# Kernel optimization log

Hardware: AMD Instinct MI355X
Metric: run time of the kernel (lower is better)

Reference implementation:

```python
import jax, jax.numpy as jnp
import numpy as np
from jax import lax

H = 128  # hidden_size


def lstm_last_h(x, w_ih, w_hh, b_ih, b_hh):
    """PyTorch-style single-layer LSTM; returns final hidden state.
    x: (B, T, D). Gate order i, f, g, o. w_ih: (4H, D), w_hh: (4H, H)."""
    B = x.shape[0]
    Hh = w_hh.shape[1]
    x_proj = jnp.einsum('btd,gd->btg', x, w_ih) + b_ih + b_hh  # (B, T, 4H)

    def step(carry, xt):
        h, c = carry
        gates = xt + h @ w_hh.T
        i, f, g, o = jnp.split(gates, 4, axis=-1)
        i = jax.nn.sigmoid(i)
        f = jax.nn.sigmoid(f)
        g = jnp.tanh(g)
        o = jax.nn.sigmoid(o)
        c = f * c + i * g
        h = o * jnp.tanh(c)
        return (h, c), None

    init = (jnp.zeros((B, Hh), x.dtype), jnp.zeros((B, Hh), x.dtype))
    (h, _), _ = lax.scan(step, init, jnp.swapaxes(x_proj, 0, 1))
    return h  # (B, H)


def setup_inputs() -> dict:
    key = jax.random.key(0)
    ks = jax.random.split(key, 12)
    s = 0.05
    return {
        'x_players': jax.random.normal(ks[0], (64, 22, 128, 2), jnp.float32),
        'x_ball': jax.random.normal(ks[1], (64, 128, 2), jnp.float32),
        'p_w_ih': jax.random.normal(ks[2], (4 * H, 2), jnp.float32) * s,
        'p_w_hh': jax.random.normal(ks[3], (4 * H, H), jnp.float32) * s,
        'p_b_ih': jax.random.normal(ks[4], (4 * H,), jnp.float32) * s,
        'p_b_hh': jax.random.normal(ks[5], (4 * H,), jnp.float32) * s,
        'b_w_ih': jax.random.normal(ks[6], (4 * H, 2), jnp.float32) * s,
        'b_w_hh': jax.random.normal(ks[7], (4 * H, H), jnp.float32) * s,
        'b_b_ih': jax.random.normal(ks[8], (4 * H,), jnp.float32) * s,
        'b_b_hh': jax.random.normal(ks[9], (4 * H,), jnp.float32) * s,
        'fc_w': jax.random.normal(ks[10], (40, 2 * H), jnp.float32) * s,
        'fc_b': jax.random.normal(ks[11], (40,), jnp.float32) * s,
    }


def reference(x_players, x_ball, p_w_ih, p_w_hh, p_b_ih, p_b_hh,
              b_w_ih, b_w_hh, b_b_ih, b_b_hh, fc_w, fc_b):
    B, P, T, D = x_players.shape
    ball_h = lstm_last_h(x_ball, b_w_ih, b_w_hh, b_b_ih, b_b_hh)  # (B, H)
    # Shared player LSTM: fold players into batch (replaces per-player loop).
    ph = lstm_last_h(x_players.reshape(B * P, T, D),
                     p_w_ih, p_w_hh, p_b_ih, p_b_hh).reshape(B, P, H)
    ball_rep = jnp.broadcast_to(ball_h[:, None, :], (B, P, H))
    combined = jnp.concatenate([ph, ball_rep], axis=-1)  # (B, P, 2H)
    out = combined @ fc_w.T + fc_b  # (B, P, 40)
    return out.reshape(B, P, 20, 2)
```

## Files before the change

### kernel.cpp

```cpp
#include <hip/hip_runtime.h>


#define HDIM 128
#define TSTEPS 128
#define NPLAYER 1408
#define NSEQ 1472
#define NB 8
#define NBLK (NSEQ / NB)
#define NPBLK (NPLAYER / NB)
#define KT 5
#define BSTR 168
#define XSTR 258
#define HSTR 132

typedef _Float16 f16x8 __attribute__((ext_vector_type(8)));
typedef _Float16 f16x2 __attribute__((ext_vector_type(2)));
typedef float    f32x4 __attribute__((ext_vector_type(4)));

#define LOG2E 1.44269504f

__device__ __forceinline__ float rcp_fast(float x) { return __builtin_amdgcn_rcpf(x); }
__device__ __forceinline__ float sigmoid_f(float x) {
    return rcp_fast(1.0f + __builtin_amdgcn_exp2f(-LOG2E * x));
}
__device__ __forceinline__ float tanh_f(float x) {
    return 1.0f - 2.0f * rcp_fast(__builtin_amdgcn_exp2f(2.0f * LOG2E * x) + 1.0f);
}
__device__ __forceinline__ float dpp_xor8(float x) {
    return __int_as_float(__builtin_amdgcn_update_dpp(
        __float_as_int(x), __float_as_int(x), 0x128, 0xF, 0xF, false));
}

__global__ void __launch_bounds__(512)
__attribute__((amdgpu_waves_per_eu(2, 2)))
lstm_fc_kernel(const float* __restrict__ x_players, const float* __restrict__ x_ball,
               const float* __restrict__ p_w_ih, const float* __restrict__ p_w_hh,
               const float* __restrict__ p_b_ih, const float* __restrict__ p_b_hh,
               const float* __restrict__ b_w_ih, const float* __restrict__ b_w_hh,
               const float* __restrict__ b_b_ih, const float* __restrict__ b_b_hh,
               const float* __restrict__ fc_w, const float* __restrict__ fc_b,
               float* __restrict__ out)
{
    const int tid  = threadIdx.x;
    const int blk  = blockIdx.x;
    const int w    = tid >> 6;
    const int lane = tid & 63;
    const int nn   = lane & 15;
    const int q    = lane >> 4;

    const bool ball = (blk >= NPBLK);
    const float* w_ih = ball ? b_w_ih : p_w_ih;
    const float* w_hh = ball ? b_w_hh : p_w_hh;
    const float* bih  = ball ? b_b_ih : p_b_ih;
    const float* bhh  = ball ? b_b_hh : p_b_hh;
    const float* xg   = ball ? (x_ball    + (size_t)(blk - NPBLK) * NB * TSTEPS * 2)
                             : (x_players + (size_t)blk * NB * TSTEPS * 2);

    __shared__ __align__(16) _Float16 b_sh[2][NB * BSTR];
    __shared__ __align__(16) float x_sh[NB * XSTR];
    __shared__ __align__(16) float hbuf[NB * HSTR];
    __shared__ float vout[NB * 40];

    for (int i = tid; i < NB * 256; i += 512)
        x_sh[(i >> 8) * XSTR + (i & 255)] = xg[i];
    for (int i = tid; i < 2 * NB * BSTR / 2; i += 512)
        ((int*)b_sh)[i] = 0;

    f16x8 afr[4][KT];
    #pragma unroll
    for (int mi = 0; mi < 4; ++mi) {
        const int r = mi * HDIM + w * 16 + nn;
        const float* wr = w_hh + (size_t)r * HDIM;
        #pragma unroll
        for (int kt = 0; kt < 4; ++kt) {
            const float* p = wr + kt * 32 + q * 8;
            f16x8 a8;
            #pragma unroll
            for (int j = 0; j < 8; ++j) a8[j] = (_Float16)p[j];
            afr[mi][kt] = a8;
        }
        f16x8 a8 = {};
        if (q == 0) {
            a8[0] = (_Float16)w_ih[2 * r];
            a8[1] = (_Float16)w_ih[2 * r + 1];
            a8[2] = (_Float16)(bih[r] + bhh[r]);
        }
        afr[mi][4] = a8;
    }

    const int colh   = nn & 7;
    const int rowoff = (nn < 8) ? 0 : 2;
    const int hrow   = w * 16 + 4 * q + rowoff;
    float c0 = 0.f, c1 = 0.f;
    float h0 = 0.f, h1 = 0.f;

    __syncthreads();
    if (tid < NB) {
        _Float16* br0 = &b_sh[0][tid * BSTR];
        br0[128] = (_Float16)x_sh[tid * XSTR];
        br0[129] = (_Float16)x_sh[tid * XSTR + 1];
        br0[130] = (_Float16)1.0f;
        b_sh[1][tid * BSTR + 130] = (_Float16)1.0f;
    }
    __syncthreads();

    f16x8 bfr[KT] = {};

    auto substep = [&](int s, const _Float16* bc, _Float16* bn, bool last) {
        if (nn < 8) {
            #pragma unroll
            for (int kt = 0; kt < KT; ++kt)
                bfr[kt] = *(const f16x8*)(bc + nn * BSTR + kt * 32 + q * 8);
        }

        f32x4 acc[4];
        #pragma unroll
        for (int mi = 0; mi < 4; ++mi) acc[mi] = (f32x4){0.f, 0.f, 0.f, 0.f};
        #pragma unroll
        for (int kt = 0; kt < KT; ++kt)
            #pragma unroll
            for (int mi = 0; mi < 4; ++mi)
                acc[mi] = __builtin_amdgcn_mfma_f32_16x16x32_f16(afr[mi][kt], bfr[kt], acc[mi], 0, 0, 0);

        if (!last && tid < NB) {
            const float x0 = x_sh[tid * XSTR + 2 * (s + 1)];
            const float x1 = x_sh[tid * XSTR + 2 * (s + 1) + 1];
            *(f16x2*)&bn[tid * BSTR + 128] = (f16x2){(_Float16)x0, (_Float16)x1};
        }

        float u0[4], u1[4];
        #pragma unroll
        for (int mi = 0; mi < 4; ++mi) {
            const float r2 = dpp_xor8(acc[mi][2]);
            const float r3 = dpp_xor8(acc[mi][3]);
            u0[mi] = (nn < 8) ? acc[mi][0] : r2;
            u1[mi] = (nn < 8) ? acc[mi][1] : r3;
        }
        const float i0 = sigmoid_f(u0[0]), i1 = sigmoid_f(u1[0]);
        const float f0 = sigmoid_f(u0[1]), f1 = sigmoid_f(u1[1]);
        const float g0 = tanh_f(u0[2]),    g1 = tanh_f(u1[2]);
        const float o0 = sigmoid_f(u0[3]), o1 = sigmoid_f(u1[3]);
        c0 = __builtin_fmaf(f0, c0, i0 * g0);
        c1 = __builtin_fmaf(f1, c1, i1 * g1);
        h0 = o0 * tanh_f(c0);
        h1 = o1 * tanh_f(c1);

        if (!last) {
            *(f16x2*)&bn[colh * BSTR + hrow] = (f16x2){(_Float16)h0, (_Float16)h1};
            __syncthreads();
        }
    };

    _Float16* b0 = &b_sh[0][0];
    _Float16* b1 = &b_sh[1][0];
    #pragma unroll 1
    for (int it = 0; it < TSTEPS / 2 - 1; ++it) {
        substep(2 * it,     b0, b1, false);
        substep(2 * it + 1, b1, b0, false);
        asm volatile("" : "+a"(afr[0][0]), "+a"(afr[0][1]), "+a"(afr[0][2]), "+a"(afr[0][3]), "+a"(afr[0][4]));
        asm volatile("" : "+a"(afr[1][0]), "+a"(afr[1][1]), "+a"(afr[1][2]), "+a"(afr[1][3]), "+a"(afr[1][4]));
        asm volatile("" : "+a"(afr[2][0]), "+a"(afr[2][1]), "+a"(afr[2][2]), "+a"(afr[2][3]), "+a"(afr[2][4]));
        asm volatile("" : "+a"(afr[3][0]), "+a"(afr[3][1]), "+a"(afr[3][2]), "+a"(afr[3][3]), "+a"(afr[3][4]));
    }
    substep(126, b0, b1, false);
    substep(127, b1, b0, true);

    hbuf[colh * HSTR + hrow]     = h0;
    hbuf[colh * HSTR + hrow + 1] = h1;
    __syncthreads();

    if (!ball) {
        for (int o = tid; o < NB * 40; o += 512) {
            const int j = o / 40, row = o - j * 40;
            const float* wr = fc_w + (size_t)row * 2 * HDIM;
            const float* hp = &hbuf[j * HSTR];
            float a0 = fc_b[row], a1 = 0.f, a2 = 0.f, a3 = 0.f;
            #pragma unroll
            for (int k = 0; k < HDIM; k += 4) {
                float4 wv = *(const float4*)(wr + k);
                float4 hv = *(const float4*)(hp + k);
                a0 = __builtin_fmaf(wv.x, hv.x, a0);
                a1 = __builtin_fmaf(wv.y, hv.y, a1);
                a2 = __builtin_fmaf(wv.z, hv.z, a2);
                a3 = __builtin_fmaf(wv.w, hv.w, a3);
            }
            atomicAdd(&out[(size_t)(NB * blk + j) * 40 + row], (a0 + a1) + (a2 + a3));
        }
    } else {
        for (int o = tid; o < NB * 40; o += 512) {
            const int c = o / 40, row = o - c * 40;
            const float* wr = fc_w + (size_t)row * 2 * HDIM + HDIM;
            const float* hp = &hbuf[c * HSTR];
            float a0 = 0.f, a1 = 0.f, a2 = 0.f, a3 = 0.f;
            #pragma unroll
            for (int k = 0; k < HDIM; k += 4) {
                float4 wv = *(const float4*)(wr + k);
                float4 hv = *(const float4*)(hp + k);
                a0 = __builtin_fmaf(wv.x, hv.x, a0);
                a1 = __builtin_fmaf(wv.y, hv.y, a1);
                a2 = __builtin_fmaf(wv.z, hv.z, a2);
                a3 = __builtin_fmaf(wv.w, hv.w, a3);
            }
            vout[c * 40 + row] = (a0 + a1) + (a2 + a3);
        }
        __syncthreads();
        const int base_batch = (blk - NPBLK) * NB;
        for (int o = tid; o < NB * 22 * 40; o += 512) {
            const int c = o / 880, rem = o - c * 880;
            const int p = rem / 40, row = rem - p * 40;
            atomicAdd(&out[(size_t)((base_batch + c) * 22 + p) * 40 + row],
                      vout[c * 40 + row]);
        }
    }
}

extern "C" void kernel_launch(void* const* d_in, const int* in_sizes, int n_in,
                              void* d_out, int out_size, void* d_ws, size_t ws_size,
                              hipStream_t stream) {
    const float* x_players = (const float*)d_in[0];
    const float* x_ball    = (const float*)d_in[1];
    const float* p_w_ih    = (const float*)d_in[2];
    const float* p_w_hh    = (const float*)d_in[3];
    const float* p_b_ih    = (const float*)d_in[4];
    const float* p_b_hh    = (const float*)d_in[5];
    const float* b_w_ih    = (const float*)d_in[6];
    const float* b_w_hh    = (const float*)d_in[7];
    const float* b_b_ih    = (const float*)d_in[8];
    const float* b_b_hh    = (const float*)d_in[9];
    const float* fc_w      = (const float*)d_in[10];
    const float* fc_b      = (const float*)d_in[11];

    hipMemsetAsync(d_out, 0, (size_t)out_size * sizeof(float), stream);

    lstm_fc_kernel<<<dim3(NBLK), dim3(512), 0, stream>>>(
        x_players, x_ball, p_w_ih, p_w_hh, p_b_ih, p_b_hh,
        b_w_ih, b_w_hh, b_b_ih, b_b_hh, fc_w, fc_b, (float*)d_out);
}
```

Measured before the change: 181.5 us.

## Prescale gate weights by log2e, fuse gate activations, preload x table, drop DPP

Folds log2(e) (and 2·log2(e) for the g gate) into the recurrent and input weights and biases so activations call exp2 directly. Sigmoid and tanh are merged to share reciprocals, with the cell state kept in a scaled domain. The bias moves into the accumulator init, and all timesteps of x are staged once as an f16 table that every lane reads, which drops the per-step thread-<8 x writes and the DPP lane exchange. The trade is extra precision risk from the f16 scaling and a possible exp2 overflow on large cell values.

```diff
diff --git a/kernel.cpp b/kernel.cpp
--- a/kernel.cpp
+++ b/kernel.cpp
@@ -10,26 +10,17 @@
 #define NPBLK (NPLAYER / NB)
 #define KT 5
 #define BSTR 168
-#define XSTR 258
 #define HSTR 132
 
 typedef _Float16 f16x8 __attribute__((ext_vector_type(8)));
 typedef _Float16 f16x2 __attribute__((ext_vector_type(2)));
 typedef float    f32x4 __attribute__((ext_vector_type(4)));
 
-#define LOG2E 1.44269504f
-
-__device__ __forceinline__ float rcp_fast(float x) { return __builtin_amdgcn_rcpf(x); }
-__device__ __forceinline__ float sigmoid_f(float x) {
-    return rcp_fast(1.0f + __builtin_amdgcn_exp2f(-LOG2E * x));
-}
-__device__ __forceinline__ float tanh_f(float x) {
-    return 1.0f - 2.0f * rcp_fast(__builtin_amdgcn_exp2f(2.0f * LOG2E * x) + 1.0f);
-}
-__device__ __forceinline__ float dpp_xor8(float x) {
-    return __int_as_float(__builtin_amdgcn_update_dpp(
-        __float_as_int(x), __float_as_int(x), 0x128, 0xF, 0xF, false));
-}
+#define LOG2E 1.4426950408889634f
+#define K2    2.8853900817779268f
+
+__device__ __forceinline__ float rcp_fast(float x)  { return __builtin_amdgcn_rcpf(x); }
+__device__ __forceinline__ float exp2_fast(float x) { return __builtin_amdgcn_exp2f(x); }
 
 __global__ void __launch_bounds__(512)
 __attribute__((amdgpu_waves_per_eu(2, 2)))
@@ -57,18 +48,24 @@
                              : (x_players + (size_t)blk * NB * TSTEPS * 2);
 
     __shared__ __align__(16) _Float16 b_sh[2][NB * BSTR];
-    __shared__ __align__(16) float x_sh[NB * XSTR];
+    __shared__ __align__(4)  f16x2 x_tab[TSTEPS * NB];
     __shared__ __align__(16) float hbuf[NB * HSTR];
     __shared__ float vout[NB * 40];
 
-    for (int i = tid; i < NB * 256; i += 512)
-        x_sh[(i >> 8) * XSTR + (i & 255)] = xg[i];
     for (int i = tid; i < 2 * NB * BSTR / 2; i += 512)
         ((int*)b_sh)[i] = 0;
-
+    for (int i = tid; i < TSTEPS * NB; i += 512) {
+        const int sq = i >> 7, t = i & 127;
+        const float2 xv2 = ((const float2*)xg)[sq * TSTEPS + t];
+        x_tab[t * NB + sq] = (f16x2){(_Float16)xv2.x, (_Float16)xv2.y};
+    }
+
+    const int rowoff = (nn < 8) ? 0 : 2;
     f16x8 afr[4][KT];
+    float bias0[4], bias1[4];
     #pragma unroll
     for (int mi = 0; mi < 4; ++mi) {
+        const float sc = (mi == 2) ? K2 : LOG2E;
         const int r = mi * HDIM + w * 16 + nn;
         const float* wr = w_hh + (size_t)r * HDIM;
         #pragma unroll
@@ -76,74 +73,77 @@
             const float* p = wr + kt * 32 + q * 8;
             f16x8 a8;
             #pragma unroll
-            for (int j = 0; j < 8; ++j) a8[j] = (_Float16)p[j];
+            for (int j = 0; j < 8; ++j) a8[j] = (_Float16)(sc * p[j]);
             afr[mi][kt] = a8;
         }
         f16x8 a8 = {};
         if (q == 0) {
-            a8[0] = (_Float16)w_ih[2 * r];
-            a8[1] = (_Float16)w_ih[2 * r + 1];
-            a8[2] = (_Float16)(bih[r] + bhh[r]);
+            a8[0] = (_Float16)(sc * w_ih[2 * r]);
+            a8[1] = (_Float16)(sc * w_ih[2 * r + 1]);
         }
         afr[mi][4] = a8;
-    }
-
-    const int colh   = nn & 7;
-    const int rowoff = (nn < 8) ? 0 : 2;
-    const int hrow   = w * 16 + 4 * q + rowoff;
+        const int rb = mi * HDIM + w * 16 + 4 * q + rowoff;
+        bias0[mi] = sc * (bih[rb] + bhh[rb]);
+        bias1[mi] = sc * (bih[rb + 1] + bhh[rb + 1]);
+    }
+
+    const int colh = nn & 7;
+    const int hrow = w * 16 + 4 * q + rowoff;
     float c0 = 0.f, c1 = 0.f;
     float h0 = 0.f, h1 = 0.f;
 
     __syncthreads();
-    if (tid < NB) {
-        _Float16* br0 = &b_sh[0][tid * BSTR];
-        br0[128] = (_Float16)x_sh[tid * XSTR];
-        br0[129] = (_Float16)x_sh[tid * XSTR + 1];
-        br0[130] = (_Float16)1.0f;
-        b_sh[1][tid * BSTR + 130] = (_Float16)1.0f;
-    }
-    __syncthreads();
-
-    f16x8 bfr[KT] = {};
+
+    f16x8 bx = {};
 
     auto substep = [&](int s, const _Float16* bc, _Float16* bn, bool last) {
-        if (nn < 8) {
-            #pragma unroll
-            for (int kt = 0; kt < KT; ++kt)
-                bfr[kt] = *(const f16x8*)(bc + nn * BSTR + kt * 32 + q * 8);
+        f16x8 bfr[4];
+        const _Float16* bp = bc + colh * BSTR + q * 8;
+        #pragma unroll
+        for (int kt = 0; kt < 4; ++kt)
+            bfr[kt] = *(const f16x8*)(bp + kt * 32);
+        {
+            const f16x2 xv = x_tab[s * NB + colh];
+            bx[0] = xv[0]; bx[1] = xv[1];
         }
 
         f32x4 acc[4];
         #pragma unroll
-        for (int mi = 0; mi < 4; ++mi) acc[mi] = (f32x4){0.f, 0.f, 0.f, 0.f};
-        #pragma unroll
-        for (int kt = 0; kt < KT; ++kt)
+        for (int mi = 0; mi < 4; ++mi)
+            acc[mi] = (f32x4){bias0[mi], bias1[mi], bias0[mi], bias1[mi]};
+        #pragma unroll
+        for (int kt = 0; kt < 4; ++kt)
             #pragma unroll
             for (int mi = 0; mi < 4; ++mi)
                 acc[mi] = __builtin_amdgcn_mfma_f32_16x16x32_f16(afr[mi][kt], bfr[kt], acc[mi], 0, 0, 0);
-
-        if (!last && tid < NB) {
-            const float x0 = x_sh[tid * XSTR + 2 * (s + 1)];
-            const float x1 = x_sh[tid * XSTR + 2 * (s + 1) + 1];
-            *(f16x2*)&bn[tid * BSTR + 128] = (f16x2){(_Float16)x0, (_Float16)x1};
-        }
+        #pragma unroll
+        for (int mi = 0; mi < 4; ++mi)
+            acc[mi] = __builtin_amdgcn_mfma_f32_16x16x32_f16(afr[mi][4], bx, acc[mi], 0, 0, 0);
 
         float u0[4], u1[4];
         #pragma unroll
         for (int mi = 0; mi < 4; ++mi) {
-            const float r2 = dpp_xor8(acc[mi][2]);
-            const float r3 = dpp_xor8(acc[mi][3]);
-            u0[mi] = (nn < 8) ? acc[mi][0] : r2;
-            u1[mi] = (nn < 8) ? acc[mi][1] : r3;
-        }
-        const float i0 = sigmoid_f(u0[0]), i1 = sigmoid_f(u1[0]);
-        const float f0 = sigmoid_f(u0[1]), f1 = sigmoid_f(u1[1]);
-        const float g0 = tanh_f(u0[2]),    g1 = tanh_f(u1[2]);
-        const float o0 = sigmoid_f(u0[3]), o1 = sigmoid_f(u1[3]);
-        c0 = __builtin_fmaf(f0, c0, i0 * g0);
-        c1 = __builtin_fmaf(f1, c1, i1 * g1);
-        h0 = o0 * tanh_f(c0);
-        h1 = o1 * tanh_f(c1);
+            u0[mi] = (nn < 8) ? acc[mi][0] : acc[mi][2];
+            u1[mi] = (nn < 8) ? acc[mi][1] : acc[mi][3];
+        }
+
+        const float A0 = exp2_fast(-u0[0]), A1 = exp2_fast(-u1[0]);
+        const float F0 = exp2_fast(-u0[1]), F1 = exp2_fast(-u1[1]);
+        const float G0 = exp2_fast( u0[2]), G1 = exp2_fast( u1[2]);
+        const float O0 = exp2_fast(-u0[3]), O1 = exp2_fast(-u1[3]);
+        const float r0 = rcp_fast((1.0f + A0) * (G0 + 1.0f));
+        const float r1 = rcp_fast((1.0f + A1) * (G1 + 1.0f));
+        const float ig0 = __builtin_fmaf(G0, K2, -K2) * r0;
+        const float ig1 = __builtin_fmaf(G1, K2, -K2) * r1;
+        const float f0 = rcp_fast(1.0f + F0);
+        const float f1 = rcp_fast(1.0f + F1);
+        c0 = __builtin_fmaf(f0, c0, ig0);
+        c1 = __builtin_fmaf(f1, c1, ig1);
+        const float C0 = exp2_fast(c0), C1 = exp2_fast(c1);
+        const float rr0 = rcp_fast((C0 + 1.0f) * (1.0f + O0));
+        const float rr1 = rcp_fast((C1 + 1.0f) * (1.0f + O1));
+        h0 = (C0 - 1.0f) * rr0;
+        h1 = (C1 - 1.0f) * rr1;
 
         if (!last) {
             *(f16x2*)&bn[colh * BSTR + hrow] = (f16x2){(_Float16)h0, (_Float16)h1};
```

Result: faster. 168.2 us (-7.3%).
